# Kernel optimization log

Hardware: AMD Instinct MI355X
Metric: run time of the kernel (lower is better)

The kernel has to match this reference:

```python
import jax, jax.numpy as jnp
import numpy as np

BS, G, L, D = 64, 64, 100, 64


def setup_inputs() -> dict:
    key = jax.random.key(0)
    ks = jax.random.split(key, 12)
    s = 1.0 / np.sqrt(D)
    return {
        "seqs": jax.random.normal(ks[0], (BS, G, L, D), dtype=jnp.float32),
        "lens": jax.random.randint(ks[1], (BS, G, 1), 1, L + 1, dtype=jnp.int32),
        "W1": jax.random.normal(ks[2], (D, D), dtype=jnp.float32) * s,
        "W2": jax.random.normal(ks[3], (D, D), dtype=jnp.float32) * s,
        "W3": jax.random.normal(ks[4], (D, D), dtype=jnp.float32) * s,
        "b": jnp.zeros((D,), dtype=jnp.float32),
        "p": jax.random.normal(ks[5], (D,), dtype=jnp.float32) * s,
        "Wq": jax.random.normal(ks[6], (D, 2 * D), dtype=jnp.float32) * s,
        "Wl_0": jax.random.normal(ks[7], (2 * D, 2 * D), dtype=jnp.float32) * s,
        "bl_0": jnp.zeros((2 * D,), dtype=jnp.float32),
        "Wl_1": jax.random.normal(ks[8], (2 * D, 2 * D), dtype=jnp.float32) * s,
        "bl_1": jnp.zeros((2 * D,), dtype=jnp.float32),
    }


def reference(seqs, lens, W1, W2, W3, b, p, Wq, Wl_0, bl_0, Wl_1, bl_1):
    # seqs: [bs, g, L, d]; lens: [bs, g, 1]
    V_last = jnp.einsum('bgd,de->bge', seqs[:, :, -1, :], W1)[:, :, None, :]
    V_seq = jnp.einsum('bgld,de->bgle', seqs, W2)
    avg = jnp.sum(seqs, axis=-2) / lens.astype(jnp.float32)  # [bs, g, d]
    V_avg = jnp.einsum('bgd,de->bge', avg, W3)[:, :, None, :]
    emb = jnp.einsum('bgld,d->bgl', V_last + V_seq + V_avg + b, p)  # [bs, g, L]
    attn = jax.nn.softmax(emb, axis=-1)
    weighted = jnp.einsum('bgl,bgld->bgd', attn, seqs)  # attention-weighted pooling
    h0 = weighted @ Wq  # [bs, g, 2d]
    h = jax.nn.relu(h0 @ Wl_0 + bl_0)
    h = jax.nn.relu(h @ Wl_1 + bl_1)
    return h0 + h  # residual
```

## Files before the change

### kernel.cpp

```cpp
#include <hip/hip_runtime.h>
#include <cstddef>

#define LL 100
#define DD 64
#define NG 4

typedef float vf4 __attribute__((ext_vector_type(4)));

template<int CTRL>
__device__ __forceinline__ float dpp_add(float x) {
    int s = __builtin_amdgcn_update_dpp(0, __float_as_int(x), CTRL, 0xF, 0xF, true);
    return x + __int_as_float(s);
}

__device__ __forceinline__ float sum16_all(float x) {
    x = dpp_add<0xB1>(x);
    x = dpp_add<0x4E>(x);
    x = dpp_add<0x141>(x);
    x = dpp_add<0x140>(x);
    return x;
}

__device__ __forceinline__ vf4 nt_load4(const float* p) {
    return __builtin_nontemporal_load((const vf4*)p);
}

__global__ __launch_bounds__(256, 4) void seq_encoder_fused(
    const float* __restrict__ seqs,
    const float* __restrict__ W2,  const float* __restrict__ p,
    const float* __restrict__ Wq,  const float* __restrict__ Wl0,
    const float* __restrict__ bl0, const float* __restrict__ Wl1,
    const float* __restrict__ bl1, float* __restrict__ out)
{
    __shared__ __align__(16) float s_q2[DD];
    __shared__ __align__(16) float s_w[NG][DD];
    __shared__ __align__(16) float s_p[2][NG][2 * DD];
    __shared__ __align__(16) float s_h0[NG][2 * DD];
    __shared__ __align__(16) float s_h1[NG][2 * DD];

    const int tid = threadIdx.x;
    const int r = tid >> 6;
    const int lane = tid & 63;

    {
        const int row = tid >> 2, part = tid & 3;
        const float* wrow = W2 + row * DD + part * 16;
        const float* pp = p + part * 16;
        float s = 0.f;
        #pragma unroll
        for (int e = 0; e < 16; ++e) s += wrow[e] * pp[e];
        s += __shfl_down(s, 2);
        s += __shfl_down(s, 1);
        if (part == 0) s_q2[row] = s;
    }
    __syncthreads();

    const int rg = lane >> 4;
    const int cb = lane & 15;
    const float4 q2v = *(const float4*)&s_q2[cb * 4];

    const int gi = blockIdx.x * NG + r;
    const float* Sp = seqs + (size_t)gi * (LL * DD) + (rg * 16 + cb) * 4;

    float z = 0.f;
    float wx = 0.f, wy = 0.f, wzv = 0.f, ww = 0.f;

    vf4 buf[3][5];
    #pragma unroll
    for (int j = 0; j < 5; ++j) buf[0][j] = nt_load4(Sp + j * 256);
    #pragma unroll
    for (int j = 0; j < 5; ++j) buf[1][j] = nt_load4(Sp + (5 + j) * 256);

    #pragma unroll
    for (int b = 0; b < 5; ++b) {
        if (b + 2 < 5) {
            #pragma unroll
            for (int j = 0; j < 5; ++j)
                buf[(b + 2) % 3][j] = nt_load4(Sp + ((b + 2) * 5 + j) * 256);
        }
        #pragma unroll
        for (int j = 0; j < 5; ++j) {
            vf4 x = buf[b % 3][j];
            float t = x.x * q2v.x + x.y * q2v.y + x.z * q2v.z + x.w * q2v.w;
            t = sum16_all(t);
            float e = __expf(t);
            z += e;
            wx  += e * x.x; wy += e * x.y;
            wzv += e * x.z; ww += e * x.w;
        }
    }

    z   += __shfl_xor(z, 16);   z   += __shfl_xor(z, 32);
    wx  += __shfl_xor(wx, 16);  wx  += __shfl_xor(wx, 32);
    wy  += __shfl_xor(wy, 16);  wy  += __shfl_xor(wy, 32);
    wzv += __shfl_xor(wzv, 16); wzv += __shfl_xor(wzv, 32);
    ww  += __shfl_xor(ww, 16);  ww  += __shfl_xor(ww, 32);

    const float invz = 1.f / z;
    if (rg == 0) {
        float4 o;
        o.x = wx * invz; o.y = wy * invz; o.z = wzv * invz; o.w = ww * invz;
        *(float4*)&s_w[r][cb * 4] = o;
    }
    __syncthreads();

    const int jt = tid & 127;
    const int hf = tid >> 7;
    const int g0 = 2 * hf;

    {
        float p0 = 0.f, p1 = 0.f, p2 = 0.f, p3 = 0.f;
        const int k0 = hf * 32;
        for (int k = k0; k < k0 + 32; ++k) {
            float wv = Wq[k * (2 * DD) + jt];
            p0 += s_w[0][k] * wv; p1 += s_w[1][k] * wv;
            p2 += s_w[2][k] * wv; p3 += s_w[3][k] * wv;
        }
        s_p[hf][0][jt] = p0; s_p[hf][1][jt] = p1;
        s_p[hf][2][jt] = p2; s_p[hf][3][jt] = p3;
    }
    __syncthreads();
    {
        s_h0[g0][jt]     = s_p[0][g0][jt]     + s_p[1][g0][jt];
        s_h0[g0 + 1][jt] = s_p[0][g0 + 1][jt] + s_p[1][g0 + 1][jt];
    }
    __syncthreads();

    {
        float p0 = 0.f, p1 = 0.f, p2 = 0.f, p3 = 0.f;
        const int k0 = hf * 64;
        for (int k = k0; k < k0 + 64; ++k) {
            float wv = Wl0[k * (2 * DD) + jt];
            p0 += s_h0[0][k] * wv; p1 += s_h0[1][k] * wv;
            p2 += s_h0[2][k] * wv; p3 += s_h0[3][k] * wv;
        }
        s_p[hf][0][jt] = p0; s_p[hf][1][jt] = p1;
        s_p[hf][2][jt] = p2; s_p[hf][3][jt] = p3;
    }
    __syncthreads();
    {
        float bv = bl0[jt];
        s_h1[g0][jt]     = fmaxf(s_p[0][g0][jt]     + s_p[1][g0][jt]     + bv, 0.f);
        s_h1[g0 + 1][jt] = fmaxf(s_p[0][g0 + 1][jt] + s_p[1][g0 + 1][jt] + bv, 0.f);
    }
    __syncthreads();

    {
        float p0 = 0.f, p1 = 0.f, p2 = 0.f, p3 = 0.f;
        const int k0 = hf * 64;
        for (int k = k0; k < k0 + 64; ++k) {
            float wv = Wl1[k * (2 * DD) + jt];
            p0 += s_h1[0][k] * wv; p1 += s_h1[1][k] * wv;
            p2 += s_h1[2][k] * wv; p3 += s_h1[3][k] * wv;
        }
        s_p[hf][0][jt] = p0; s_p[hf][1][jt] = p1;
        s_p[hf][2][jt] = p2; s_p[hf][3][jt] = p3;
    }
    __syncthreads();
    {
        float bv = bl1[jt];
        float oa = fmaxf(s_p[0][g0][jt]     + s_p[1][g0][jt]     + bv, 0.f);
        float ob = fmaxf(s_p[0][g0 + 1][jt] + s_p[1][g0 + 1][jt] + bv, 0.f);
        const size_t gbase = (size_t)blockIdx.x * NG;
        out[(gbase + g0) * (2 * DD) + jt]     = s_h0[g0][jt]     + oa;
        out[(gbase + g0 + 1) * (2 * DD) + jt] = s_h0[g0 + 1][jt] + ob;
    }
}

extern "C" void kernel_launch(void* const* d_in, const int* in_sizes, int n_in,
                              void* d_out, int out_size, void* d_ws, size_t ws_size,
                              hipStream_t stream) {
    const float* seqs = (const float*)d_in[0];
    const float* W2   = (const float*)d_in[3];
    const float* p    = (const float*)d_in[6];
    const float* Wq   = (const float*)d_in[7];
    const float* Wl0  = (const float*)d_in[8];
    const float* bl0  = (const float*)d_in[9];
    const float* Wl1  = (const float*)d_in[10];
    const float* bl1  = (const float*)d_in[11];
    float* out = (float*)d_out;

    const int n_groups = 64 * 64;
    seq_encoder_fused<<<n_groups / NG, 256, 0, stream>>>(
        seqs, W2, p, Wq, Wl0, bl0, Wl1, bl1, out);
}
```

Before: 172.0 us.

## Stream sequence rows through an LDS ring via direct global-to-LDS DMA loads

Replaces the register-buffered nontemporal vector loads with global_load_lds DMA into a per-wavefront 5-slot LDS ring, using explicit vmcnt waits to keep four loads in flight. Each step then reads its float4 from LDS and does the same dot/exp/accumulate. The aim is to free registers and sustain memory parallelism, at the cost of extra LDS traffic and about 20KB more shared memory per block. That may limit occupancy under the 4-block launch bound, and the hand-written waitcnt sequencing relies on in-order completion without an LDS barrier.

Result: slower. 182.4 us (+6.0%).

```diff
diff --git a/kernel.cpp b/kernel.cpp
--- a/kernel.cpp
+++ b/kernel.cpp
@@ -1,9 +1,13 @@
 #include <hip/hip_runtime.h>
 #include <cstddef>
+#include <cstdint>
 
 #define LL 100
 #define DD 64
 #define NG 4
+#define NPACK 25
+#define RING 5
+#define LA 4
 
 typedef float vf4 __attribute__((ext_vector_type(4)));
 
@@ -21,8 +25,18 @@
     return x;
 }
 
-__device__ __forceinline__ vf4 nt_load4(const float* p) {
-    return __builtin_nontemporal_load((const vf4*)p);
+template<int N> __device__ __forceinline__ void wait_vmcnt();
+template<> __device__ __forceinline__ void wait_vmcnt<0>() { asm volatile("s_waitcnt vmcnt(0)" ::: "memory"); }
+template<> __device__ __forceinline__ void wait_vmcnt<1>() { asm volatile("s_waitcnt vmcnt(1)" ::: "memory"); }
+template<> __device__ __forceinline__ void wait_vmcnt<2>() { asm volatile("s_waitcnt vmcnt(2)" ::: "memory"); }
+template<> __device__ __forceinline__ void wait_vmcnt<3>() { asm volatile("s_waitcnt vmcnt(3)" ::: "memory"); }
+template<> __device__ __forceinline__ void wait_vmcnt<4>() { asm volatile("s_waitcnt vmcnt(4)" ::: "memory"); }
+
+__device__ __forceinline__ void lds_dma16(const float* g, float* l) {
+    __builtin_amdgcn_global_load_lds(
+        (const __attribute__((address_space(1))) void*)g,
+        (__attribute__((address_space(3))) void*)l,
+        16, 0, 0);
 }
 
 __global__ __launch_bounds__(256, 4) void seq_encoder_fused(
@@ -33,6 +47,7 @@
     const float* __restrict__ bl1, float* __restrict__ out)
 {
     __shared__ __align__(16) float s_q2[DD];
+    __shared__ __align__(16) float s_ring[NG][RING][256];
     __shared__ __align__(16) float s_w[NG][DD];
     __shared__ __align__(16) float s_p[2][NG][2 * DD];
     __shared__ __align__(16) float s_h0[NG][2 * DD];
@@ -60,34 +75,34 @@
     const float4 q2v = *(const float4*)&s_q2[cb * 4];
 
     const int gi = blockIdx.x * NG + r;
-    const float* Sp = seqs + (size_t)gi * (LL * DD) + (rg * 16 + cb) * 4;
+    const float* Sp = seqs + (size_t)gi * (LL * DD) + lane * 4;
+    float* ring = &s_ring[r][0][0];
 
     float z = 0.f;
     float wx = 0.f, wy = 0.f, wzv = 0.f, ww = 0.f;
 
-    vf4 buf[3][5];
     #pragma unroll
-    for (int j = 0; j < 5; ++j) buf[0][j] = nt_load4(Sp + j * 256);
+    for (int j = 0; j < LA; ++j)
+        lds_dma16(Sp + j * 256, ring + j * 256);
+
     #pragma unroll
-    for (int j = 0; j < 5; ++j) buf[1][j] = nt_load4(Sp + (5 + j) * 256);
-
-    #pragma unroll
-    for (int b = 0; b < 5; ++b) {
-        if (b + 2 < 5) {
-            #pragma unroll
-            for (int j = 0; j < 5; ++j)
-                buf[(b + 2) % 3][j] = nt_load4(Sp + ((b + 2) * 5 + j) * 256);
-        }
-        #pragma unroll
-        for (int j = 0; j < 5; ++j) {
-            vf4 x = buf[b % 3][j];
-            float t = x.x * q2v.x + x.y * q2v.y + x.z * q2v.z + x.w * q2v.w;
-            t = sum16_all(t);
-            float e = __expf(t);
-            z += e;
-            wx  += e * x.x; wy += e * x.y;
-            wzv += e * x.z; ww += e * x.w;
-        }
+    for (int j = 0; j < NPACK; ++j) {
+        if (j + LA < NPACK)
+            lds_dma16(Sp + (j + LA) * 256, ring + ((j + LA) % RING) * 256);
+        const int rem = NPACK - 1 - j;
+        if      (rem >= LA) wait_vmcnt<LA>();
+        else if (rem == 3)  wait_vmcnt<3>();
+        else if (rem == 2)  wait_vmcnt<2>();
+        else if (rem == 1)  wait_vmcnt<1>();
+        else                wait_vmcnt<0>();
+
+        vf4 x = *(const vf4*)(ring + (j % RING) * 256 + lane * 4);
+        float t = x.x * q2v.x + x.y * q2v.y + x.z * q2v.z + x.w * q2v.w;
+        t = sum16_all(t);
+        float e = __expf(t);
+        z += e;
+        wx  += e * x.x; wy += e * x.y;
+        wzv += e * x.z; ww += e * x.w;
     }
 
     z   += __shfl_xor(z, 16);   z   += __shfl_xor(z, 32);
```

## Interleave block-wide contiguous loads across waves with per-group partial softmax accumulators

Applied to the files above, without the earlier changes.

The streaming loop now has the four waves read the block's four contiguous sequence groups in interleaved 1 KB chunks rather than each wave reading its own group. Each wave keeps partial softmax sums and weighted accumulators for all four groups, splitting rows that straddle a group boundary. The partials are then combined through shared memory. Per-iteration barriers keep the waves in lockstep so their accesses coalesce into one contiguous stream. The cost is more registers, extra accumulate work per row, and extra barriers.

After: 171.3 us. Within noise of the previous version (-0.4%).

```diff
diff --git a/kernel.cpp b/kernel.cpp
--- a/kernel.cpp
+++ b/kernel.cpp
@@ -33,6 +33,8 @@
     const float* __restrict__ bl1, float* __restrict__ out)
 {
     __shared__ __align__(16) float s_q2[DD];
+    __shared__ __align__(16) float s_zpart[NG][NG];
+    __shared__ __align__(16) float s_wpart[NG][NG][DD];
     __shared__ __align__(16) float s_w[NG][DD];
     __shared__ __align__(16) float s_p[2][NG][2 * DD];
     __shared__ __align__(16) float s_h0[NG][2 * DD];
@@ -59,48 +61,84 @@
     const int cb = lane & 15;
     const float4 q2v = *(const float4*)&s_q2[cb * 4];
 
-    const int gi = blockIdx.x * NG + r;
-    const float* Sp = seqs + (size_t)gi * (LL * DD) + (rg * 16 + cb) * 4;
-
-    float z = 0.f;
-    float wx = 0.f, wy = 0.f, wzv = 0.f, ww = 0.f;
+    const float* Sp = seqs + (size_t)blockIdx.x * (NG * LL * DD) + r * 256 + lane * 4;
+
+    float z[NG]  = {0.f, 0.f, 0.f, 0.f};
+    vf4   acc[NG];
+    #pragma unroll
+    for (int g = 0; g < NG; ++g) acc[g] = (vf4){0.f, 0.f, 0.f, 0.f};
 
     vf4 buf[3][5];
     #pragma unroll
-    for (int j = 0; j < 5; ++j) buf[0][j] = nt_load4(Sp + j * 256);
-    #pragma unroll
-    for (int j = 0; j < 5; ++j) buf[1][j] = nt_load4(Sp + (5 + j) * 256);
+    for (int jj = 0; jj < 5; ++jj) buf[0][jj] = nt_load4(Sp + jj * 1024);
+    #pragma unroll
+    for (int jj = 0; jj < 5; ++jj) buf[1][jj] = nt_load4(Sp + (5 + jj) * 1024);
 
     #pragma unroll
     for (int b = 0; b < 5; ++b) {
+        if (b > 0) __builtin_amdgcn_s_barrier();
         if (b + 2 < 5) {
             #pragma unroll
-            for (int j = 0; j < 5; ++j)
-                buf[(b + 2) % 3][j] = nt_load4(Sp + ((b + 2) * 5 + j) * 256);
+            for (int jj = 0; jj < 5; ++jj)
+                buf[(b + 2) % 3][jj] = nt_load4(Sp + ((b + 2) * 5 + jj) * 1024);
         }
         #pragma unroll
-        for (int j = 0; j < 5; ++j) {
-            vf4 x = buf[b % 3][j];
+        for (int jj = 0; jj < 5; ++jj) {
+            const int j   = b * 5 + jj;
+            const int t0  = 4 * j;
+            const int glo = t0 / 25;
+            const int ghi = (t0 + 3) / 25;
+
+            vf4 x = buf[b % 3][jj];
             float t = x.x * q2v.x + x.y * q2v.y + x.z * q2v.z + x.w * q2v.w;
             t = sum16_all(t);
             float e = __expf(t);
-            z += e;
-            wx  += e * x.x; wy += e * x.y;
-            wzv += e * x.z; ww += e * x.w;
-        }
-    }
-
-    z   += __shfl_xor(z, 16);   z   += __shfl_xor(z, 32);
-    wx  += __shfl_xor(wx, 16);  wx  += __shfl_xor(wx, 32);
-    wy  += __shfl_xor(wy, 16);  wy  += __shfl_xor(wy, 32);
-    wzv += __shfl_xor(wzv, 16); wzv += __shfl_xor(wzv, 32);
-    ww  += __shfl_xor(ww, 16);  ww  += __shfl_xor(ww, 32);
-
-    const float invz = 1.f / z;
+
+            if (glo == ghi) {
+                z[glo] += e;
+                acc[glo].x += e * x.x; acc[glo].y += e * x.y;
+                acc[glo].z += e * x.z; acc[glo].w += e * x.w;
+            } else {
+                const float ehi = (r >= (25 * ghi - t0)) ? e : 0.f;
+                const float elo = e - ehi;
+                z[glo] += elo; z[ghi] += ehi;
+                acc[glo].x += elo * x.x; acc[glo].y += elo * x.y;
+                acc[glo].z += elo * x.z; acc[glo].w += elo * x.w;
+                acc[ghi].x += ehi * x.x; acc[ghi].y += ehi * x.y;
+                acc[ghi].z += ehi * x.z; acc[ghi].w += ehi * x.w;
+            }
+        }
+    }
+
+    #pragma unroll
+    for (int g = 0; g < NG; ++g) {
+        z[g]     += __shfl_xor(z[g], 16);     z[g]     += __shfl_xor(z[g], 32);
+        acc[g].x += __shfl_xor(acc[g].x, 16); acc[g].x += __shfl_xor(acc[g].x, 32);
+        acc[g].y += __shfl_xor(acc[g].y, 16); acc[g].y += __shfl_xor(acc[g].y, 32);
+        acc[g].z += __shfl_xor(acc[g].z, 16); acc[g].z += __shfl_xor(acc[g].z, 32);
+        acc[g].w += __shfl_xor(acc[g].w, 16); acc[g].w += __shfl_xor(acc[g].w, 32);
+    }
     if (rg == 0) {
-        float4 o;
-        o.x = wx * invz; o.y = wy * invz; o.z = wzv * invz; o.w = ww * invz;
-        *(float4*)&s_w[r][cb * 4] = o;
+        #pragma unroll
+        for (int g = 0; g < NG; ++g) {
+            *(vf4*)&s_wpart[r][g][cb * 4] = acc[g];
+            if (cb == 0) s_zpart[r][g] = z[g];
+        }
+    }
+    __syncthreads();
+
+    if (rg == 0) {
+        float zz = s_zpart[0][r] + s_zpart[1][r] + s_zpart[2][r] + s_zpart[3][r];
+        const float invz = 1.f / zz;
+        vf4 a = *(const vf4*)&s_wpart[0][r][cb * 4];
+        vf4 a1 = *(const vf4*)&s_wpart[1][r][cb * 4];
+        vf4 a2 = *(const vf4*)&s_wpart[2][r][cb * 4];
+        vf4 a3 = *(const vf4*)&s_wpart[3][r][cb * 4];
+        a.x = (a.x + a1.x + a2.x + a3.x) * invz;
+        a.y = (a.y + a1.y + a2.y + a3.y) * invz;
+        a.z = (a.z + a1.z + a2.z + a3.z) * invz;
+        a.w = (a.w + a1.w + a2.w + a3.w) * invz;
+        *(vf4*)&s_w[r][cb * 4] = a;
     }
     __syncthreads();
 
```
